# Kernel tuning notes

Hardware: AMD Instinct MI355X
Metric: run time of the kernel (lower is better)

## Reference

```python
import jax, jax.numpy as jnp
import numpy as np

N, C = 262144, 128
BN_EPS = 1e-5


def setup_inputs() -> dict:
    key = jax.random.key(0)
    ks = jax.random.split(key, 9)
    s = 1.0 / np.sqrt(C)  # torch Linear default init scale
    return {
        "x": jax.random.normal(ks[0], (N, C), dtype=jnp.float32),
        "W1": jax.random.uniform(ks[1], (C, C), jnp.float32, -s, s),
        "b1": jax.random.uniform(ks[2], (C,), jnp.float32, -s, s),
        "gamma1": jnp.ones((C,), jnp.float32),
        "beta1": jnp.zeros((C,), jnp.float32),
        "W2": jax.random.uniform(ks[3], (C, C), jnp.float32, -s, s),
        "b2": jax.random.uniform(ks[4], (C,), jnp.float32, -s, s),
        "gamma2": jnp.ones((C,), jnp.float32),
        "beta2": jnp.zeros((C,), jnp.float32),
    }


def _batchnorm(h, gamma, beta):
    # training-mode BatchNorm1d: batch mean, biased variance, eps=1e-5
    m = jnp.mean(h, axis=0)
    v = jnp.var(h, axis=0)
    return (h - m) * jax.lax.rsqrt(v + BN_EPS) * gamma + beta


def reference(x, W1, b1, gamma1, beta1, W2, b2, gamma2, beta2):
    res = x
    out = x @ W1.T + b1
    # contextNormalization: only the in-place `d -= mean` loop has effect
    # (return value is discarded in the original), i.e. mean-center over batch
    out = out - jnp.mean(out, axis=0)
    out = jax.nn.relu(_batchnorm(out, gamma1, beta1))
    out = out @ W2.T + b2
    out = out - jnp.mean(out, axis=0)
    out = jax.nn.relu(_batchnorm(out, gamma2, beta2))
    return out + res
```

## Files before the change

kernel.cpp:

```cpp
#include <hip/hip_runtime.h>
#include <hip/hip_bf16.h>

#define NROWS 262144
#define CDIM  128
#define BN_EPS 1e-5f
#define GGRID 2048
#define SPB   (NROWS / 16 / GGRID)

typedef __attribute__((ext_vector_type(8))) short bf16x8;
typedef __attribute__((ext_vector_type(4))) float f32x4;
#define LROW 136

static __device__ __forceinline__ unsigned int f2bf_rtn(float f) {
  unsigned int u = __float_as_uint(f);
  return (u + 0x7fffu + ((u >> 16) & 1u)) >> 16;
}
static __device__ __forceinline__ float bf2f(unsigned int b) {
  return __uint_as_float(b << 16);
}

template <bool NORM>
__global__ void __launch_bounds__(256, 4)
gemm_bn(const float* __restrict__ in, const float* __restrict__ W,
        const float* __restrict__ bias,
        const float* __restrict__ stats_in,
        const float* __restrict__ gamma, const float* __restrict__ beta,
        float* __restrict__ hout, float* __restrict__ stats)
{
  __shared__ __align__(16) short lds[2][2][16][LROW];

  const int tid  = threadIdx.x;
  const int lane = tid & 63;
  const int wave = tid >> 6;
  const int l15  = lane & 15;
  const int lq   = lane >> 4;
  const int wcol = wave * 32;
  const int srow = tid >> 4;
  const int sk0  = (tid & 15) * 8;

  bf16x8 bh[2][4], bl[2][4];
#pragma unroll
  for (int jt = 0; jt < 2; ++jt) {
    const float* wrow = W + (wcol + jt * 16 + l15) * CDIM;
#pragma unroll
    for (int ks = 0; ks < 4; ++ks) {
      const int k0 = ks * 32 + lq * 8;
      f32x4 w0 = *(const f32x4*)(wrow + k0);
      f32x4 w1 = *(const f32x4*)(wrow + k0 + 4);
      float wv[8] = {w0.x,w0.y,w0.z,w0.w,w1.x,w1.y,w1.z,w1.w};
#pragma unroll
      for (int e = 0; e < 8; ++e) {
        unsigned int h = f2bf_rtn(wv[e]);
        bh[jt][ks][e] = (short)h;
        bl[jt][ks][e] = (short)f2bf_rtn(wv[e] - bf2f(h));
      }
    }
  }

  float scv[8], shv[8];
  if constexpr (NORM) {
    const float inv_n = 1.0f / (float)NROWS;
#pragma unroll
    for (int e = 0; e < 8; ++e) {
      const int c = sk0 + e;
      float m  = stats_in[c] * inv_n;
      float v  = stats_in[CDIM + c] * inv_n - m * m;
      float sc = gamma[c] * rsqrtf(v + BN_EPS);
      scv[e] = sc;
      shv[e] = beta[c] - m * sc;
    }
  }

  const float bias0 = bias[wcol + l15];
  const float bias1 = bias[wcol + 16 + l15];
  float s0 = 0.f, s1 = 0.f, q0 = 0.f, q1 = 0.f;

  const int row0 = blockIdx.x * (SPB * 16);

  auto cvt_write = [&](int buf, f32x4 g0, f32x4 g1) {
    float av[8] = {g0.x,g0.y,g0.z,g0.w,g1.x,g1.y,g1.z,g1.w};
    if constexpr (NORM) {
#pragma unroll
      for (int e = 0; e < 8; ++e)
        av[e] = fmaxf(av[e] * scv[e] + shv[e], 0.f);
    }
    bf16x8 hi, lo;
#pragma unroll
    for (int e = 0; e < 8; ++e) {
      unsigned int h = f2bf_rtn(av[e]);
      hi[e] = (short)h;
      lo[e] = (short)f2bf_rtn(av[e] - bf2f(h));
    }
    *(bf16x8*)&lds[buf][0][srow][sk0] = hi;
    *(bf16x8*)&lds[buf][1][srow][sk0] = lo;
  };

  {
    const float* ap = in + (size_t)(row0 + srow) * CDIM + sk0;
    f32x4 g0 = *(const f32x4*)ap;
    f32x4 g1 = *(const f32x4*)(ap + 4);
    cvt_write(0, g0, g1);
  }
  __syncthreads();

  for (int s = 0; s < SPB; ++s) {
    const int cur = s & 1;
    const int r0 = row0 + s * 16;

    f32x4 g0 = {0,0,0,0}, g1 = {0,0,0,0};
    const bool more = (s + 1 < SPB);
    if (more) {
      const float* ap = in + (size_t)(r0 + 16 + srow) * CDIM + sk0;
      g0 = *(const f32x4*)ap;
      g1 = *(const f32x4*)(ap + 4);
    }

    f32x4 acc0 = {0.f,0.f,0.f,0.f};
    f32x4 acc1 = {0.f,0.f,0.f,0.f};
#pragma unroll
    for (int ks = 0; ks < 4; ++ks) {
      const int kc = ks * 32 + lq * 8;
      bf16x8 ah = *(const bf16x8*)&lds[cur][0][l15][kc];
      bf16x8 al = *(const bf16x8*)&lds[cur][1][l15][kc];
      acc0 = __builtin_amdgcn_mfma_f32_16x16x32_bf16(al, bh[0][ks], acc0, 0, 0, 0);
      acc0 = __builtin_amdgcn_mfma_f32_16x16x32_bf16(ah, bl[0][ks], acc0, 0, 0, 0);
      acc0 = __builtin_amdgcn_mfma_f32_16x16x32_bf16(ah, bh[0][ks], acc0, 0, 0, 0);
      acc1 = __builtin_amdgcn_mfma_f32_16x16x32_bf16(al, bh[1][ks], acc1, 0, 0, 0);
      acc1 = __builtin_amdgcn_mfma_f32_16x16x32_bf16(ah, bl[1][ks], acc1, 0, 0, 0);
      acc1 = __builtin_amdgcn_mfma_f32_16x16x32_bf16(ah, bh[1][ks], acc1, 0, 0, 0);
    }

    if (more) cvt_write(cur ^ 1, g0, g1);
    __syncthreads();

    float* op = hout + (size_t)(r0 + lq * 4) * CDIM + wcol + l15;
#pragma unroll
    for (int r = 0; r < 4; ++r) {
      float h0 = acc0[r] + bias0;
      float h1 = acc1[r] + bias1;
      s0 += h0; q0 += h0 * h0;
      s1 += h1; q1 += h1 * h1;
      op[r * CDIM] = h0;
      op[r * CDIM + 16] = h1;
    }
  }

  s0 += __shfl_xor(s0, 16); s0 += __shfl_xor(s0, 32);
  s1 += __shfl_xor(s1, 16); s1 += __shfl_xor(s1, 32);
  q0 += __shfl_xor(q0, 16); q0 += __shfl_xor(q0, 32);
  q1 += __shfl_xor(q1, 16); q1 += __shfl_xor(q1, 32);
  if (lane < 16) {
    atomicAdd(&stats[wcol + lane],             s0);
    atomicAdd(&stats[wcol + 16 + lane],        s1);
    atomicAdd(&stats[CDIM + wcol + lane],      q0);
    atomicAdd(&stats[CDIM + wcol + 16 + lane], q1);
  }
}

__global__ void __launch_bounds__(256)
finalize(const f32x4* __restrict__ h2, const f32x4* __restrict__ xin,
         const float* __restrict__ stats, const float* __restrict__ gamma,
         const float* __restrict__ beta, f32x4* __restrict__ outp)
{
  const int tid0 = blockIdx.x * blockDim.x + threadIdx.x;
  const int c0 = (tid0 * 4) & (CDIM - 1);

  const float inv_n = 1.0f / (float)NROWS;
  float sc[4], sh[4];
#pragma unroll
  for (int e = 0; e < 4; ++e) {
    const int c = c0 + e;
    float m = stats[c] * inv_n;
    float v = stats[CDIM + c] * inv_n - m * m;
    float s = gamma[c] * rsqrtf(v + BN_EPS);
    sc[e] = s;
    sh[e] = beta[c] - m * s;
  }

  const int n4 = NROWS * CDIM / 4;
  const int GR = gridDim.x * blockDim.x;
  for (int base = tid0; base < n4; base += GR * 4) {
    f32x4 h[4], xv[4], o[4];
#pragma unroll
    for (int u = 0; u < 4; ++u) {
      h[u]  = h2[base + u * GR];
      xv[u] = __builtin_nontemporal_load(&xin[base + u * GR]);
    }
#pragma unroll
    for (int u = 0; u < 4; ++u) {
      o[u].x = fmaxf(h[u].x * sc[0] + sh[0], 0.f) + xv[u].x;
      o[u].y = fmaxf(h[u].y * sc[1] + sh[1], 0.f) + xv[u].y;
      o[u].z = fmaxf(h[u].z * sc[2] + sh[2], 0.f) + xv[u].z;
      o[u].w = fmaxf(h[u].w * sc[3] + sh[3], 0.f) + xv[u].w;
    }
#pragma unroll
    for (int u = 0; u < 4; ++u)
      __builtin_nontemporal_store(o[u], &outp[base + u * GR]);
  }
}

extern "C" void kernel_launch(void* const* d_in, const int* in_sizes, int n_in,
                              void* d_out, int out_size, void* d_ws, size_t ws_size,
                              hipStream_t stream) {
  (void)in_sizes; (void)n_in; (void)out_size; (void)ws_size;
  const float* x   = (const float*)d_in[0];
  const float* W1  = (const float*)d_in[1];
  const float* b1  = (const float*)d_in[2];
  const float* g1  = (const float*)d_in[3];
  const float* be1 = (const float*)d_in[4];
  const float* W2  = (const float*)d_in[5];
  const float* b2  = (const float*)d_in[6];
  const float* g2  = (const float*)d_in[7];
  const float* be2 = (const float*)d_in[8];

  float* hbuf   = (float*)d_out;
  float* stats1 = (float*)d_ws;
  float* stats2 = stats1 + 256;

  (void)hipMemsetAsync(d_ws, 0, 2048, stream);

  gemm_bn<false><<<GGRID, 256, 0, stream>>>(x, W1, b1, nullptr, nullptr, nullptr,
                                            hbuf, stats1);
  gemm_bn<true><<<GGRID, 256, 0, stream>>>(hbuf, W2, b2, stats1, g1, be1,
                                           hbuf, stats2);
  finalize<<<2048, 256, 0, stream>>>((const f32x4*)hbuf, (const f32x4*)x,
                                     stats2, g2, be2, (f32x4*)d_out);
}
```

Before: 471.4 us.

## Process 32-row strips per GEMM step and replace stat atomics with per-block partials

Each GEMM block now handles two 16-row sub-tiles per pipeline step over half as many blocks, which halves the per-step barrier count and increases MFMA work per weight-register load. The global float atomics for BatchNorm statistics are replaced by per-block partial sums written to workspace and reduced by a new bn_stats kernel that also precomputes scale and shift. This removes the memset and the repeated per-thread scale/shift computation, and the finalize grid is doubled. The cost is two extra kernel launches and larger LDS/register use per block, which may reduce occupancy.

```diff
diff --git a/kernel.cpp b/kernel.cpp
--- a/kernel.cpp
+++ b/kernel.cpp
@@ -4,8 +4,9 @@
 #define NROWS 262144
 #define CDIM  128
 #define BN_EPS 1e-5f
-#define GGRID 2048
-#define SPB   (NROWS / 16 / GGRID)
+#define GGRID 1024
+#define SROWS 32
+#define SPB   (NROWS / SROWS / GGRID)
 
 typedef __attribute__((ext_vector_type(8))) short bf16x8;
 typedef __attribute__((ext_vector_type(4))) float f32x4;
@@ -23,11 +24,10 @@
 __global__ void __launch_bounds__(256, 4)
 gemm_bn(const float* __restrict__ in, const float* __restrict__ W,
         const float* __restrict__ bias,
-        const float* __restrict__ stats_in,
-        const float* __restrict__ gamma, const float* __restrict__ beta,
-        float* __restrict__ hout, float* __restrict__ stats)
+        const float* __restrict__ scsh_in,
+        float* __restrict__ hout, float* __restrict__ part)
 {
-  __shared__ __align__(16) short lds[2][2][16][LROW];
+  __shared__ __align__(16) short lds[2][2][SROWS][LROW];
 
   const int tid  = threadIdx.x;
   const int lane = tid & 63;
@@ -59,15 +59,10 @@
 
   float scv[8], shv[8];
   if constexpr (NORM) {
-    const float inv_n = 1.0f / (float)NROWS;
 #pragma unroll
     for (int e = 0; e < 8; ++e) {
-      const int c = sk0 + e;
-      float m  = stats_in[c] * inv_n;
-      float v  = stats_in[CDIM + c] * inv_n - m * m;
-      float sc = gamma[c] * rsqrtf(v + BN_EPS);
-      scv[e] = sc;
-      shv[e] = beta[c] - m * sc;
+      scv[e] = scsh_in[sk0 + e];
+      shv[e] = scsh_in[CDIM + sk0 + e];
     }
   }
 
@@ -75,9 +70,9 @@
   const float bias1 = bias[wcol + 16 + l15];
   float s0 = 0.f, s1 = 0.f, q0 = 0.f, q1 = 0.f;
 
-  const int row0 = blockIdx.x * (SPB * 16);
-
-  auto cvt_write = [&](int buf, f32x4 g0, f32x4 g1) {
+  const int row0 = blockIdx.x * (SPB * SROWS);
+
+  auto cvt_write = [&](int buf, int lrow, f32x4 g0, f32x4 g1) {
     float av[8] = {g0.x,g0.y,g0.z,g0.w,g1.x,g1.y,g1.z,g1.w};
     if constexpr (NORM) {
 #pragma unroll
@@ -91,57 +86,74 @@
       hi[e] = (short)h;
       lo[e] = (short)f2bf_rtn(av[e] - bf2f(h));
     }
-    *(bf16x8*)&lds[buf][0][srow][sk0] = hi;
-    *(bf16x8*)&lds[buf][1][srow][sk0] = lo;
+    *(bf16x8*)&lds[buf][0][lrow][sk0] = hi;
+    *(bf16x8*)&lds[buf][1][lrow][sk0] = lo;
   };
 
   {
-    const float* ap = in + (size_t)(row0 + srow) * CDIM + sk0;
-    f32x4 g0 = *(const f32x4*)ap;
-    f32x4 g1 = *(const f32x4*)(ap + 4);
-    cvt_write(0, g0, g1);
+    const float* a0 = in + (size_t)(row0 + srow) * CDIM + sk0;
+    const float* a1 = in + (size_t)(row0 + 16 + srow) * CDIM + sk0;
+    f32x4 g0 = *(const f32x4*)a0, g1 = *(const f32x4*)(a0 + 4);
+    f32x4 g2 = *(const f32x4*)a1, g3 = *(const f32x4*)(a1 + 4);
+    cvt_write(0, srow, g0, g1);
+    cvt_write(0, srow + 16, g2, g3);
   }
   __syncthreads();
 
   for (int s = 0; s < SPB; ++s) {
     const int cur = s & 1;
-    const int r0 = row0 + s * 16;
-
-    f32x4 g0 = {0,0,0,0}, g1 = {0,0,0,0};
+    const int r0 = row0 + s * SROWS;
+
+    f32x4 g0 = {0,0,0,0}, g1 = {0,0,0,0}, g2 = {0,0,0,0}, g3 = {0,0,0,0};
     const bool more = (s + 1 < SPB);
     if (more) {
-      const float* ap = in + (size_t)(r0 + 16 + srow) * CDIM + sk0;
-      g0 = *(const f32x4*)ap;
-      g1 = *(const f32x4*)(ap + 4);
-    }
-
-    f32x4 acc0 = {0.f,0.f,0.f,0.f};
-    f32x4 acc1 = {0.f,0.f,0.f,0.f};
-#pragma unroll
-    for (int ks = 0; ks < 4; ++ks) {
-      const int kc = ks * 32 + lq * 8;
-      bf16x8 ah = *(const bf16x8*)&lds[cur][0][l15][kc];
-      bf16x8 al = *(const bf16x8*)&lds[cur][1][l15][kc];
-      acc0 = __builtin_amdgcn_mfma_f32_16x16x32_bf16(al, bh[0][ks], acc0, 0, 0, 0);
-      acc0 = __builtin_amdgcn_mfma_f32_16x16x32_bf16(ah, bl[0][ks], acc0, 0, 0, 0);
-      acc0 = __builtin_amdgcn_mfma_f32_16x16x32_bf16(ah, bh[0][ks], acc0, 0, 0, 0);
-      acc1 = __builtin_amdgcn_mfma_f32_16x16x32_bf16(al, bh[1][ks], acc1, 0, 0, 0);
-      acc1 = __builtin_amdgcn_mfma_f32_16x16x32_bf16(ah, bl[1][ks], acc1, 0, 0, 0);
-      acc1 = __builtin_amdgcn_mfma_f32_16x16x32_bf16(ah, bh[1][ks], acc1, 0, 0, 0);
-    }
-
-    if (more) cvt_write(cur ^ 1, g0, g1);
+      const float* a0 = in + (size_t)(r0 + SROWS + srow) * CDIM + sk0;
+      const float* a1 = in + (size_t)(r0 + SROWS + 16 + srow) * CDIM + sk0;
+      g0 = *(const f32x4*)a0; g1 = *(const f32x4*)(a0 + 4);
+      g2 = *(const f32x4*)a1; g3 = *(const f32x4*)(a1 + 4);
+    }
+
+    f32x4 acc[2][2];
+#pragma unroll
+    for (int st = 0; st < 2; ++st)
+#pragma unroll
+      for (int jt = 0; jt < 2; ++jt)
+        acc[st][jt] = (f32x4){0.f,0.f,0.f,0.f};
+
+#pragma unroll
+    for (int st = 0; st < 2; ++st) {
+#pragma unroll
+      for (int ks = 0; ks < 4; ++ks) {
+        const int kc = ks * 32 + lq * 8;
+        bf16x8 ah = *(const bf16x8*)&lds[cur][0][st * 16 + l15][kc];
+        bf16x8 al = *(const bf16x8*)&lds[cur][1][st * 16 + l15][kc];
+        acc[st][0] = __builtin_amdgcn_mfma_f32_16x16x32_bf16(al, bh[0][ks], acc[st][0], 0, 0, 0);
+        acc[st][0] = __builtin_amdgcn_mfma_f32_16x16x32_bf16(ah, bl[0][ks], acc[st][0], 0, 0, 0);
+        acc[st][0] = __builtin_amdgcn_mfma_f32_16x16x32_bf16(ah, bh[0][ks], acc[st][0], 0, 0, 0);
+        acc[st][1] = __builtin_amdgcn_mfma_f32_16x16x32_bf16(al, bh[1][ks], acc[st][1], 0, 0, 0);
+        acc[st][1] = __builtin_amdgcn_mfma_f32_16x16x32_bf16(ah, bl[1][ks], acc[st][1], 0, 0, 0);
+        acc[st][1] = __builtin_amdgcn_mfma_f32_16x16x32_bf16(ah, bh[1][ks], acc[st][1], 0, 0, 0);
+      }
+    }
+
+    if (more) {
+      cvt_write(cur ^ 1, srow, g0, g1);
+      cvt_write(cur ^ 1, srow + 16, g2, g3);
+    }
     __syncthreads();
 
-    float* op = hout + (size_t)(r0 + lq * 4) * CDIM + wcol + l15;
-#pragma unroll
-    for (int r = 0; r < 4; ++r) {
-      float h0 = acc0[r] + bias0;
-      float h1 = acc1[r] + bias1;
-      s0 += h0; q0 += h0 * h0;
-      s1 += h1; q1 += h1 * h1;
-      op[r * CDIM] = h0;
-      op[r * CDIM + 16] = h1;
+#pragma unroll
+    for (int st = 0; st < 2; ++st) {
+      float* op = hout + (size_t)(r0 + st * 16 + lq * 4) * CDIM + wcol + l15;
+#pragma unroll
+      for (int r = 0; r < 4; ++r) {
+        float h0 = acc[st][0][r] + bias0;
+        float h1 = acc[st][1][r] + bias1;
+        s0 += h0; q0 += h0 * h0;
+        s1 += h1; q1 += h1 * h1;
+        op[r * CDIM] = h0;
+        op[r * CDIM + 16] = h1;
+      }
     }
   }
 
@@ -149,32 +161,56 @@
   s1 += __shfl_xor(s1, 16); s1 += __shfl_xor(s1, 32);
   q0 += __shfl_xor(q0, 16); q0 += __shfl_xor(q0, 32);
   q1 += __shfl_xor(q1, 16); q1 += __shfl_xor(q1, 32);
+  float* pb = part + (size_t)blockIdx.x * 256;
   if (lane < 16) {
-    atomicAdd(&stats[wcol + lane],             s0);
-    atomicAdd(&stats[wcol + 16 + lane],        s1);
-    atomicAdd(&stats[CDIM + wcol + lane],      q0);
-    atomicAdd(&stats[CDIM + wcol + 16 + lane], q1);
+    pb[wcol + lane]              = s0;
+    pb[wcol + 16 + lane]         = s1;
+    pb[CDIM + wcol + lane]       = q0;
+    pb[CDIM + wcol + 16 + lane]  = q1;
+  }
+}
+
+__global__ void __launch_bounds__(256)
+bn_stats(const float* __restrict__ part, const float* __restrict__ gamma,
+         const float* __restrict__ beta, float* __restrict__ scsh)
+{
+  const int c = blockIdx.x;
+  const int t = threadIdx.x;
+  float s = 0.f, q = 0.f;
+  for (int b = t; b < GGRID; b += 256) {
+    s += part[(size_t)b * 256 + c];
+    q += part[(size_t)b * 256 + CDIM + c];
+  }
+  __shared__ float rs[256], rq[256];
+  rs[t] = s; rq[t] = q;
+  __syncthreads();
+#pragma unroll
+  for (int off = 128; off >= 1; off >>= 1) {
+    if (t < off) { rs[t] += rs[t + off]; rq[t] += rq[t + off]; }
+    __syncthreads();
+  }
+  if (t == 0) {
+    const float inv_n = 1.0f / (float)NROWS;
+    float m  = rs[0] * inv_n;
+    float v  = rq[0] * inv_n - m * m;
+    float sc = gamma[c] * rsqrtf(v + BN_EPS);
+    scsh[c]        = sc;
+    scsh[CDIM + c] = beta[c] - m * sc;
   }
 }
 
 __global__ void __launch_bounds__(256)
 finalize(const f32x4* __restrict__ h2, const f32x4* __restrict__ xin,
-         const float* __restrict__ stats, const float* __restrict__ gamma,
-         const float* __restrict__ beta, f32x4* __restrict__ outp)
+         const float* __restrict__ scsh, f32x4* __restrict__ outp)
 {
   const int tid0 = blockIdx.x * blockDim.x + threadIdx.x;
   const int c0 = (tid0 * 4) & (CDIM - 1);
 
-  const float inv_n = 1.0f / (float)NROWS;
   float sc[4], sh[4];
 #pragma unroll
   for (int e = 0; e < 4; ++e) {
-    const int c = c0 + e;
-    float m = stats[c] * inv_n;
-    float v = stats[CDIM + c] * inv_n - m * m;
-    float s = gamma[c] * rsqrtf(v + BN_EPS);
-    sc[e] = s;
-    sh[e] = beta[c] - m * s;
+    sc[e] = scsh[c0 + e];
+    sh[e] = scsh[CDIM + c0 + e];
   }
 
   const int n4 = NROWS * CDIM / 4;
@@ -213,16 +249,16 @@
   const float* g2  = (const float*)d_in[7];
   const float* be2 = (const float*)d_in[8];
 
-  float* hbuf   = (float*)d_out;
-  float* stats1 = (float*)d_ws;
-  float* stats2 = stats1 + 256;
-
-  (void)hipMemsetAsync(d_ws, 0, 2048, stream);
-
-  gemm_bn<false><<<GGRID, 256, 0, stream>>>(x, W1, b1, nullptr, nullptr, nullptr,
-                                            hbuf, stats1);
-  gemm_bn<true><<<GGRID, 256, 0, stream>>>(hbuf, W2, b2, stats1, g1, be1,
-                                           hbuf, stats2);
-  finalize<<<2048, 256, 0, stream>>>((const f32x4*)hbuf, (const f32x4*)x,
-                                     stats2, g2, be2, (f32x4*)d_out);
-}
+  float* hbuf  = (float*)d_out;
+  float* part1 = (float*)d_ws;
+  float* part2 = part1 + (size_t)GGRID * 256;
+  float* scsh1 = part2 + (size_t)GGRID * 256;
+  float* scsh2 = scsh1 + 256;
+
+  gemm_bn<false><<<GGRID, 256, 0, stream>>>(x, W1, b1, nullptr, hbuf, part1);
+  bn_stats<<<CDIM, 256, 0, stream>>>(part1, g1, be1, scsh1);
+  gemm_bn<true><<<GGRID, 256, 0, stream>>>(hbuf, W2, b2, scsh1, hbuf, part2);
+  bn_stats<<<CDIM, 256, 0, stream>>>(part2, g2, be2, scsh2);
+  finalize<<<4096, 256, 0, stream>>>((const f32x4*)hbuf, (const f32x4*)x,
+                                     scsh2, (f32x4*)d_out);
+}
```

Result: faster. 456.7 us (-3.1%).
